# Kernel optimization log

Hardware: AMD Instinct MI355X
Metric: run time of the kernel (lower is better)

Reference implementation:

```python
import jax, jax.numpy as jnp
import numpy as np

T, N, C = 1024, 4, 4
RADIUS, COMPRESSION = 256, 1
TAU = 2.0  # LIF filter time constant (LIF_Filter source unavailable; exponential leaky integrator assumed)


def _build_delay():
    # Mirrors JeffressFilter.__init__ delay construction exactly.
    neg = np.arange(-RADIUS, 0, COMPRESSION, dtype=np.int64)
    pos = np.arange(RADIUS, 0, -COMPRESSION, dtype=np.int64)[::-1]
    _d = np.concatenate([neg, pos]).reshape(-1, 1)            # (D_out, 1)
    delay = np.maximum(np.concatenate([_d, -_d], axis=1), 0)  # relu -> (D_out, 2)
    return jnp.asarray(delay, dtype=jnp.int32)


def setup_inputs() -> dict:
    key = jax.random.key(0)
    k1, k2 = jax.random.split(key)
    x = jax.random.normal(k1, (T, N, C, 2), dtype=jnp.float32)
    delay = _build_delay()                                   # (D_out, 2) int
    d_out = delay.shape[0]                                   # 512
    # get_weight(1.0, 10.0, compression) source unavailable; stand-in float vector per output channel
    weight = jax.random.normal(k2, (d_out,), dtype=jnp.float32)
    return {"x": x, "weight": weight, "delay": delay}


def _lif_filter(x):
    # Leaky integrator over time axis 0: v[t] = exp(-1/tau) * v[t-1] + x[t]
    decay = jnp.asarray(np.exp(-1.0 / TAU), dtype=x.dtype)

    def step(v, xt):
        v = decay * v + xt
        return v, v

    _, y = jax.lax.scan(step, jnp.zeros(x.shape[1:], x.dtype), x)
    return y  # (T, N, C, 2)


def reference(x, weight, delay):
    Tlen = x.shape[0]
    y = _lif_filter(x)                                       # (T, N, C, 2)

    t = jnp.arange(Tlen, dtype=jnp.int32)
    # SpikeDelay.forward: mask rows t >= T - delay to 0, then gather at (t - delay) % T.
    # Equivalent post-gather: out[t] = y[t - delay] if t >= delay else 0 (zero-padded shift).
    t_idx = (t[:, None, None] - delay[None]) % Tlen          # (T, D_out, 2)
    i_idx = jnp.arange(2, dtype=jnp.int32)[None, None, :]    # broadcast over (T, D_out, 2)
    yt = jnp.moveaxis(y, -1, 1)                              # (T, 2, N, C)
    gathered = yt[t_idx, i_idx]                              # (T, D_out, 2, N, C)
    mask = t[:, None, None] >= delay[None]                   # (T, D_out, 2)
    out = jnp.where(mask[..., None, None], gathered, 0.0)
    out = out.sum(axis=2)                                    # sum over in_features=2 -> (T, D_out, N, C)
    out = jnp.moveaxis(out, 1, -1)                           # (T, N, C, D_out)
    return out * weight                                      # scale per output channel
```

## Files before the change

kernel.cpp:

```cpp
#include <hip/hip_runtime.h>


#define T_LEN  1024
#define D_OUT  512
#define NC     16
#define PAD    256
#define ROW    (PAD + T_LEN)
#define YB_OFF (NC * ROW)

__global__ __launch_bounds__(64) void lif_scan_kernel(const float* __restrict__ x,
                                                      float* __restrict__ ws) {
    const int tid = threadIdx.x;
    const int b   = blockIdx.x;

    #pragma unroll
    for (int k = 0; k < 4; ++k) {
        const int id = (b * 64 + tid) * 4 + k;
        const int r  = id >> 8;
        const int c  = id & 255;
        ws[r * ROW + c] = 0.0f;
    }

    const int ch    = tid & 31;
    const int chunk = b * 2 + (tid >> 5);
    const int nc    = ch >> 1;
    const int i     = ch & 1;
    float* row = ws + (i ? YB_OFF : 0) + nc * ROW + PAD;

    const int   t0    = chunk * 16;
    const float decay = 0.60653065971263342f;

    float v = 0.0f;
    #pragma unroll 16
    for (int k = 0; k < 64; ++k) {
        const int t = t0 - 64 + k;
        const float xv = (t >= 0) ? x[t * 32 + ch] : 0.0f;
        v = decay * v + xv;
    }
    #pragma unroll
    for (int k = 0; k < 16; ++k) {
        const int t = t0 + k;
        v = decay * v + x[t * 32 + ch];
        row[t] = v;
    }
}

__global__ __launch_bounds__(256) void jeffress_kernel(const float* __restrict__ ws,
                                                       const float* __restrict__ w,
                                                       const int2* __restrict__ delay,
                                                       float* __restrict__ out) {
    const int wid  = blockIdx.x * 4 + (threadIdx.x >> 6);
    const int lane = threadIdx.x & 63;
    const int t    = wid >> 4;
    const int nc   = wid & 15;

    const float* A = ws + nc * ROW + PAD;
    const float* B = A + YB_OFF;
    float* orow = out + ((size_t)(t * NC + nc)) * D_OUT;

    #pragma unroll
    for (int g = 0; g < 8; ++g) {
        const int d  = g * 64 + lane;
        const int2 e = delay[d];
        const float u0 = A[t - e.x];
        const float u1 = B[t - e.y];
        orow[d] = w[d] * (u0 + u1);
    }
}

extern "C" void kernel_launch(void* const* d_in, const int* in_sizes, int n_in,
                              void* d_out, int out_size, void* d_ws, size_t ws_size,
                              hipStream_t stream) {
    const float* x      = (const float*)d_in[0];
    const float* weight = (const float*)d_in[1];
    const int*   delay  = (const int*)d_in[2];
    float* out = (float*)d_out;
    float* ws  = (float*)d_ws;

    lif_scan_kernel<<<32, 64, 0, stream>>>(x, ws);

    jeffress_kernel<<<(T_LEN * NC) / 4, 256, 0, stream>>>(
        ws, weight, (const int2*)delay, (float4*)out ? (float*)out : (float*)out);
}
```

Baseline: 78.32 us.

## Fuse LIF scan into Jeffress kernel with per-block shared-memory window

Replaces the two-kernel pipeline (global scan into workspace, then gather) with one kernel. Each block recomputes the LIF-filtered window it needs (256+16 samples for two channels) into shared memory, using a 64-step warm-up that approximates the decayed history. It then serves 16 timesteps from LDS, with delay and weight values held in registers across those timesteps. This removes a kernel launch and the global workspace round trip, at the cost of redundant scan work in every block and a serial scan done by a single wave before the block barrier.

```diff
diff --git a/kernel.cpp b/kernel.cpp
--- a/kernel.cpp
+++ b/kernel.cpp
@@ -4,67 +4,68 @@
 #define T_LEN  1024
 #define D_OUT  512
 #define NC     16
-#define PAD    256
-#define ROW    (PAD + T_LEN)
-#define YB_OFF (NC * ROW)
+#define TT     16
+#define WIN    (256 + TT)
+#define WARM   64
 
-__global__ __launch_bounds__(64) void lif_scan_kernel(const float* __restrict__ x,
-                                                      float* __restrict__ ws) {
+__global__ __launch_bounds__(256) void jeffress_fused(const float* __restrict__ x,
+                                                      const float* __restrict__ w,
+                                                      const int2* __restrict__ delay,
+                                                      float* __restrict__ out) {
+    __shared__ float yl[2][WIN];
+
+    const int bid = blockIdx.x;
+    const int nc  = bid & 15;
+    const int t0  = (bid >> 4) * TT;
     const int tid = threadIdx.x;
-    const int b   = blockIdx.x;
+    const int lane = tid & 63;
+    const int wv   = tid >> 6;
+
+    int2  e[8];
+    float wr[8];
+    #pragma unroll
+    for (int g = 0; g < 8; ++g) {
+        const int d = g * 64 + lane;
+        e[g]  = delay[d];
+        wr[g] = w[d];
+    }
+
+    if (tid < 64) {
+        const int c  = tid >> 1;
+        const int i  = tid & 1;
+        const int ch = nc * 2 + i;
+        const int p0 = c * 9;
+        const int tb = t0 - 256 + p0;
+        const float decay = 0.60653065971263342f;
+
+        float v = 0.0f;
+        #pragma unroll 16
+        for (int j = 0; j < WARM; ++j) {
+            const int t = tb - WARM + j;
+            v = decay * v + ((t >= 0 && t < T_LEN) ? x[t * 32 + ch] : 0.0f);
+        }
+        #pragma unroll
+        for (int k = 0; k < 9; ++k) {
+            const int t = tb + k;
+            v = decay * v + ((t >= 0 && t < T_LEN) ? x[t * 32 + ch] : 0.0f);
+            const int p = p0 + k;
+            if (p < WIN) yl[i][p] = v;
+        }
+    }
+    __syncthreads();
 
     #pragma unroll
     for (int k = 0; k < 4; ++k) {
-        const int id = (b * 64 + tid) * 4 + k;
-        const int r  = id >> 8;
-        const int c  = id & 255;
-        ws[r * ROW + c] = 0.0f;
-    }
-
-    const int ch    = tid & 31;
-    const int chunk = b * 2 + (tid >> 5);
-    const int nc    = ch >> 1;
-    const int i     = ch & 1;
-    float* row = ws + (i ? YB_OFF : 0) + nc * ROW + PAD;
-
-    const int   t0    = chunk * 16;
-    const float decay = 0.60653065971263342f;
-
-    float v = 0.0f;
-    #pragma unroll 16
-    for (int k = 0; k < 64; ++k) {
-        const int t = t0 - 64 + k;
-        const float xv = (t >= 0) ? x[t * 32 + ch] : 0.0f;
-        v = decay * v + xv;
-    }
-    #pragma unroll
-    for (int k = 0; k < 16; ++k) {
-        const int t = t0 + k;
-        v = decay * v + x[t * 32 + ch];
-        row[t] = v;
-    }
-}
-
-__global__ __launch_bounds__(256) void jeffress_kernel(const float* __restrict__ ws,
-                                                       const float* __restrict__ w,
-                                                       const int2* __restrict__ delay,
-                                                       float* __restrict__ out) {
-    const int wid  = blockIdx.x * 4 + (threadIdx.x >> 6);
-    const int lane = threadIdx.x & 63;
-    const int t    = wid >> 4;
-    const int nc   = wid & 15;
-
-    const float* A = ws + nc * ROW + PAD;
-    const float* B = A + YB_OFF;
-    float* orow = out + ((size_t)(t * NC + nc)) * D_OUT;
-
-    #pragma unroll
-    for (int g = 0; g < 8; ++g) {
-        const int d  = g * 64 + lane;
-        const int2 e = delay[d];
-        const float u0 = A[t - e.x];
-        const float u1 = B[t - e.y];
-        orow[d] = w[d] * (u0 + u1);
+        const int ts   = wv * 4 + k;
+        const int t    = t0 + ts;
+        const int base = ts + 256;
+        float* orow = out + ((size_t)(t * NC + nc)) * D_OUT;
+        #pragma unroll
+        for (int g = 0; g < 8; ++g) {
+            const float u0 = yl[0][base - e[g].x];
+            const float u1 = yl[1][base - e[g].y];
+            orow[g * 64 + lane] = wr[g] * (u0 + u1);
+        }
     }
 }
 
@@ -75,10 +76,8 @@
     const float* weight = (const float*)d_in[1];
     const int*   delay  = (const int*)d_in[2];
     float* out = (float*)d_out;
-    float* ws  = (float*)d_ws;
+    (void)d_ws; (void)ws_size;
 
-    lif_scan_kernel<<<32, 64, 0, stream>>>(x, ws);
-
-    jeffress_kernel<<<(T_LEN * NC) / 4, 256, 0, stream>>>(
-        ws, weight, (const int2*)delay, (float4*)out ? (float*)out : (float*)out);
+    const int nblocks = (T_LEN / TT) * NC;
+    jeffress_fused<<<nblocks, 256, 0, stream>>>(x, weight, (const int2*)delay, out);
 }
```

New measurement: 77.29 us. About the same (-1.3%).
